# Optimization experiments

Hardware: AMD Instinct MI355X
Metric: run time of the kernel (lower is better)

The kernel has to match this reference:

```python
import jax, jax.numpy as jnp
import numpy as np

E = 8        # n_routed_experts
K = 4        # num_experts_per_tok
T = 1024     # tokens
H = 1024     # hidden_size
I = 1408     # moe_intermediate_size


def setup_inputs() -> dict:
    key = jax.random.key(0)
    ks = jax.random.split(key, 6)
    hidden_states = jax.random.normal(ks[0], (T, H), jnp.float32)
    rw = jax.random.uniform(ks[1], (T, K), jnp.float32)
    router_weights = rw / jnp.sum(rw, axis=-1, keepdims=True)  # normalized top-k router weights
    selected_experts = jax.random.randint(ks[2], (T, K), 0, E, jnp.int32)
    gate_w = jax.random.normal(ks[3], (E, H, I), jnp.float32) * (H ** -0.5)  # lecun_normal-ish
    up_w = jax.random.normal(ks[4], (E, H, I), jnp.float32) * (H ** -0.5)
    down_w = jax.random.normal(ks[5], (E, I, H), jnp.float32) * (I ** -0.5)
    return {
        'hidden_states': hidden_states,
        'router_weights': router_weights,
        'gate_w': gate_w,
        'up_w': up_w,
        'down_w': down_w,
        'selected_experts': selected_experts,
    }


def _grouped_matmul(x, w, seg):
    # x: [m, k] tokens sorted by expert; w: [E, k, n]; seg: [m] expert id per row.
    # Grouped GEMM expressed as E masked GEMMs (fixed small loop over experts);
    # a custom kernel would do true variable-group-size grouped GEMM.
    out = jnp.zeros((x.shape[0], w.shape[-1]), x.dtype)
    for e in range(w.shape[0]):
        out = out + jnp.where((seg == e)[:, None], x, jnp.zeros((), x.dtype)) @ w[e]
    return out


def reference(hidden_states, router_weights, gate_w, up_w, down_w, selected_experts):
    t, k = selected_experts.shape
    flat = selected_experts.ravel()                       # [t*k]
    hs = jnp.repeat(hidden_states, k, axis=0)             # [t*k, H]
    sort_idx = jnp.argsort(flat)                          # dispatch: sort tokens by expert
    seg = flat[sort_idx]
    xs = hs[sort_idx]
    gate = _grouped_matmul(xs, gate_w, seg)               # [t*k, I]
    up = _grouped_matmul(xs, up_w, seg)                   # [t*k, I]
    h = jax.nn.silu(gate) * up                            # fused SwiGLU
    down = _grouped_matmul(h, down_w, seg)                # [t*k, H]
    unsort = jnp.argsort(sort_idx)                        # scatter back to token order
    out = down[unsort].reshape(t, k, -1)
    return jnp.sum(out * router_weights[..., None], axis=1)  # weighted combine [t, H]
```

## Files before the change

kernel.cpp:

```cpp
#include <hip/hip_runtime.h>
#include <hip/hip_bf16.h>
#include <cstdint>
#include <cstddef>

#define NE 8
#define NT 1024
#define NK 4
#define NH 1024
#define NI 1408
#define NA (NT * NK)
#define BM 128
#define MAXTILES 40
#define PADSLOTS 5120

typedef short short8 __attribute__((ext_vector_type(8)));
typedef float f32x4 __attribute__((ext_vector_type(4)));
typedef float f4v __attribute__((ext_vector_type(4)));
typedef unsigned short u16;

#define WS_HDR   0
#define WS_SORT  1024
#define WS_XBF   21504
#define WS_GT    2118656
#define WS_UT    25187328
#define WS_DT    48256000
#define WS_HB    71324672

__device__ __forceinline__ u16 f2b(float f) {
  union { float f; uint32_t u; } c; c.f = f;
  uint32_t u = c.u;
  return (u16)((u + 0x7FFFu + ((u >> 16) & 1u)) >> 16);
}

__device__ __forceinline__ void llds16(const void* g, void* l) {
  __builtin_amdgcn_global_load_lds(
      (const __attribute__((address_space(1))) void*)g,
      (__attribute__((address_space(3))) void*)l, 16, 0, 0);
}

__device__ __forceinline__ void transcvt_stripe(const float* __restrict__ src,
                                                u16* __restrict__ dst,
                                                int K, int N, int k0, int n0,
                                                u16* smem, int tid) {
  u16 (*t2)[64][64] = (u16(*)[64][64])smem;
  int r = tid >> 4, c = tid & 15;
  f4v v[2][4];
#pragma unroll
  for (int t = 0; t < 2; ++t)
#pragma unroll
    for (int i = 0; i < 4; ++i)
      v[t][i] = __builtin_nontemporal_load(
          (const f4v*)&src[(size_t)(k0 + r + 16 * i) * N + n0 + t * 64 + c * 4]);
#pragma unroll
  for (int t = 0; t < 2; ++t)
#pragma unroll
    for (int i = 0; i < 4; ++i) {
      ushort4 o;
      o.x = f2b(v[t][i].x); o.y = f2b(v[t][i].y); o.z = f2b(v[t][i].z); o.w = f2b(v[t][i].w);
      int row = r + 16 * i;
      int sc = (c * 4) ^ (row & 56);
      *(ushort4*)&t2[t][row][sc] = o;
    }
  __syncthreads();
#pragma unroll
  for (int t = 0; t < 2; ++t)
#pragma unroll
    for (int i = 0; i < 2; ++i) {
      int idx = i * 256 + tid;
      int n = idx >> 3, kc = idx & 7;
      int cs = n ^ (kc * 8);
      u16 o[8];
#pragma unroll
      for (int j = 0; j < 8; ++j) o[j] = t2[t][kc * 8 + j][cs];
      *(short8*)&dst[(size_t)(n0 + t * 64 + n) * K + k0 + kc * 8] = *(const short8*)o;
    }
}

__global__ __launch_bounds__(256) void k1_prep(
    const float* __restrict__ gw, const float* __restrict__ uw, const float* __restrict__ dw,
    const float* __restrict__ hs, const int* __restrict__ sel,
    u16* __restrict__ gT, u16* __restrict__ uT, u16* __restrict__ dT, u16* __restrict__ xbf,
    int* __restrict__ hdr, int* __restrict__ sorted, float* __restrict__ outz) {
  int tid = threadIdx.x;
  int y = blockIdx.y;
  if (y == 24) {
    for (int i = blockIdx.x * 256 + tid; i * 4 < NT * NH; i += 176 * 256) {
      f4v v = __builtin_nontemporal_load((const f4v*)&hs[i * 4]);
      ushort4 o;
      o.x = f2b(v.x); o.y = f2b(v.y); o.z = f2b(v.z); o.w = f2b(v.w);
      *(ushort4*)&xbf[i * 4] = o;
    }
    return;
  }
  if (y == 25) {
    int x = blockIdx.x;
    if (x >= 1 && x <= 64) {
      int base = (x - 1) * 16384;
      f4v z = {0.f, 0.f, 0.f, 0.f};
#pragma unroll
      for (int i = 0; i < 16; ++i)
        *(f4v*)&outz[base + (i * 256 + tid) * 4] = z;
      return;
    }
    if (x != 0) return;
    __shared__ int cnt[NE], fill[NE], poff_s[NE + 1];
    if (tid < NE) { cnt[tid] = 0; fill[tid] = 0; }
    __syncthreads();
    for (int i = tid; i < NA; i += 256) atomicAdd(&cnt[sel[i]], 1);
    __syncthreads();
    if (tid == 0) {
      int off = 0, nt = 0;
      for (int e = 0; e < NE; ++e) {
        poff_s[e] = off;
        int tiles = (cnt[e] + BM - 1) / BM;
        for (int j = 0; j < tiles; ++j) { hdr[32 + nt] = e; hdr[80 + nt] = off + j * BM; ++nt; }
        off += tiles * BM;
      }
      poff_s[NE] = off;
      hdr[17] = nt;
      for (int e = 0; e < NE; ++e) hdr[e] = cnt[e];
      for (int e = 0; e <= NE; ++e) hdr[8 + e] = poff_s[e];
    }
    __syncthreads();
    for (int i = tid; i < PADSLOTS; i += 256) sorted[i] = -1;
    __syncthreads();
    for (int i = tid; i < NA; i += 256) {
      int e = sel[i];
      int p = atomicAdd(&fill[e], 1);
      sorted[poff_s[e] + p] = i;
    }
    return;
  }
  __shared__ u16 smem[2 * 64 * 64];
  if (y < 16) {
    int tensor = y >> 3, e = y & 7;
    const float* src = ((tensor == 0) ? gw : uw) + (size_t)e * NH * NI;
    u16* dst = ((tensor == 0) ? gT : uT) + (size_t)e * NH * NI;
    int nb = blockIdx.x % 11, kb = blockIdx.x / 11;
    transcvt_stripe(src, dst, NH, NI, kb * 64, nb * 128, smem, tid);
  } else {
    int e = y - 16;
    const float* src = dw + (size_t)e * NI * NH;
    u16* dst = dT + (size_t)e * NI * NH;
    int nb = blockIdx.x % 8, kb = blockIdx.x / 8;
    transcvt_stripe(src, dst, NI, NH, kb * 64, nb * 128, smem, tid);
  }
}

__global__ __launch_bounds__(256, 2) void k2_gemm1(
    const u16* __restrict__ xbf, const u16* __restrict__ gT, const u16* __restrict__ uT,
    u16* __restrict__ hbuf, const int* __restrict__ hdr, const int* __restrict__ sorted) {
  __shared__ u16 smem[24576];
  int b = blockIdx.x;
  int tid = threadIdx.x;

  int tile = b % 40;
  if (tile >= hdr[17]) return;
  int e = hdr[32 + tile];
  int slot0 = hdr[80 + tile];
  int n0 = (b / 40) * 128;

  u16* sA  = smem;
  u16* sBg = smem + 8192;
  u16* sBu = smem + 16384;

  const u16* aptr[4];
  for (int s = 0; s < 4; ++s) {
    int idx = s * 256 + tid;
    int row = idx >> 3, c = idx & 7;
    int kc = c ^ (row & 7);
    int as = sorted[slot0 + row];
    int trow = (as >= 0) ? (as >> 2) : 0;
    aptr[s] = xbf + (size_t)trow * NH + kc * 8;
  }
  const u16 *bgp[4], *bup[4];
  for (int s = 0; s < 4; ++s) {
    int idx = s * 256 + tid;
    int n = idx >> 3, c = idx & 7;
    int kc = c ^ (n & 7);
    size_t o = ((size_t)e * NI + n0 + n) * NH + kc * 8;
    bgp[s] = gT + o; bup[s] = uT + o;
  }

  int lane = tid & 63, wave = tid >> 6;
  int wm = wave >> 1, wn = wave & 1;
  int l15 = lane & 15, quad = lane >> 4;
  int sw = l15 & 7;

  f32x4 accg[4][4] = {}; f32x4 accu[4][4] = {};

  for (int kt = 0; kt < NH / 64; ++kt) {
    int ko = kt * 64;
    for (int s = 0; s < 4; ++s) llds16(aptr[s] + ko, &sA[(s * 256 + tid) * 8]);
    for (int s = 0; s < 4; ++s) llds16(bgp[s] + ko, &sBg[(s * 256 + tid) * 8]);
    for (int s = 0; s < 4; ++s) llds16(bup[s] + ko, &sBu[(s * 256 + tid) * 8]);
    __syncthreads();
    for (int ks = 0; ks < 2; ++ks) {
      int pos = ((ks * 4 + quad) ^ sw) * 8;
      short8 av[4], bg[4], bu[4];
      for (int mf = 0; mf < 4; ++mf)
        av[mf] = *(const short8*)&sA[(wm * 64 + mf * 16 + l15) * 64 + pos];
      for (int nf = 0; nf < 4; ++nf) {
        bg[nf] = *(const short8*)&sBg[(wn * 64 + nf * 16 + l15) * 64 + pos];
        bu[nf] = *(const short8*)&sBu[(wn * 64 + nf * 16 + l15) * 64 + pos];
      }
      for (int mf = 0; mf < 4; ++mf)
        for (int nf = 0; nf < 4; ++nf) {
          accg[mf][nf] = __builtin_amdgcn_mfma_f32_16x16x32_bf16(av[mf], bg[nf], accg[mf][nf], 0, 0, 0);
          accu[mf][nf] = __builtin_amdgcn_mfma_f32_16x16x32_bf16(av[mf], bu[nf], accu[mf][nf], 0, 0, 0);
        }
    }
    __syncthreads();
  }

  for (int mf = 0; mf < 4; ++mf)
    for (int nf = 0; nf < 4; ++nf)
      for (int r = 0; r < 4; ++r) {
        int row = wm * 64 + mf * 16 + quad * 4 + r;
        int col = n0 + wn * 64 + nf * 16 + l15;
        float g2 = accg[mf][nf][r], u = accu[mf][nf][r];
        float hv = (g2 / (1.f + __expf(-g2))) * u;
        hbuf[(size_t)(slot0 + row) * NI + col] = f2b(hv);
      }
}

__global__ __launch_bounds__(256, 4) void k3_gemm2(
    const u16* __restrict__ hbuf, const u16* __restrict__ dT,
    const float* __restrict__ rw, float* __restrict__ out,
    const int* __restrict__ hdr, const int* __restrict__ sorted) {
  int tile = blockIdx.x;
  if (tile >= hdr[17]) return;
  int e = hdr[32 + tile];
  int slot0 = hdr[80 + tile];
  int n0 = blockIdx.y * 128;
  int tid = threadIdx.x;

  __shared__ u16 sA[128 * 64];
  __shared__ u16 sB[128 * 64];

  const u16 *ap[4], *bp[4];
  for (int s = 0; s < 4; ++s) {
    int idx = s * 256 + tid;
    int r = idx >> 3, c = idx & 7;
    int kc = c ^ (r & 7);
    ap[s] = hbuf + (size_t)(slot0 + r) * NI + kc * 8;
    bp[s] = dT + ((size_t)e * NH + n0 + r) * NI + kc * 8;
  }

  int lane = tid & 63, wave = tid >> 6;
  int wm = wave >> 1, wn = wave & 1;
  int l15 = lane & 15, quad = lane >> 4;
  int sw = l15 & 7;

  f32x4 acc[4][4] = {};

  for (int kt = 0; kt < NI / 64; ++kt) {
    int ko = kt * 64;
    for (int s = 0; s < 4; ++s) llds16(ap[s] + ko, &sA[(s * 256 + tid) * 8]);
    for (int s = 0; s < 4; ++s) llds16(bp[s] + ko, &sB[(s * 256 + tid) * 8]);
    __syncthreads();
    for (int ks = 0; ks < 2; ++ks) {
      int pos = ((ks * 4 + quad) ^ sw) * 8;
      short8 av[4], bv[4];
      for (int mf = 0; mf < 4; ++mf)
        av[mf] = *(const short8*)&sA[(wm * 64 + mf * 16 + l15) * 64 + pos];
      for (int nf = 0; nf < 4; ++nf)
        bv[nf] = *(const short8*)&sB[(wn * 64 + nf * 16 + l15) * 64 + pos];
      for (int mf = 0; mf < 4; ++mf)
        for (int nf = 0; nf < 4; ++nf)
          acc[mf][nf] = __builtin_amdgcn_mfma_f32_16x16x32_bf16(av[mf], bv[nf], acc[mf][nf], 0, 0, 0);
    }
    __syncthreads();
  }

  for (int mf = 0; mf < 4; ++mf) {
    int rowb = wm * 64 + mf * 16 + quad * 4;
    for (int r = 0; r < 4; ++r) {
      int as = sorted[slot0 + rowb + r];
      if (as < 0) continue;
      float w = rw[as];
      float* orow = out + (size_t)(as >> 2) * NH + n0 + wn * 64;
      for (int nf = 0; nf < 4; ++nf)
        atomicAdd(&orow[nf * 16 + l15], w * acc[mf][nf][r]);
    }
  }
}

extern "C" void kernel_launch(void* const* d_in, const int* in_sizes, int n_in,
                              void* d_out, int out_size, void* d_ws, size_t ws_size,
                              hipStream_t stream) {
  const float* hs  = (const float*)d_in[0];
  const float* rw  = (const float*)d_in[1];
  const float* gw  = (const float*)d_in[2];
  const float* uw  = (const float*)d_in[3];
  const float* dw  = (const float*)d_in[4];
  const int*   sel = (const int*)d_in[5];
  float* out = (float*)d_out;

  char* ws = (char*)d_ws;
  int*  hdr    = (int*)(ws + WS_HDR);
  int*  sorted = (int*)(ws + WS_SORT);
  u16*  xbf    = (u16*)(ws + WS_XBF);
  u16*  gT     = (u16*)(ws + WS_GT);
  u16*  uT     = (u16*)(ws + WS_UT);
  u16*  dT     = (u16*)(ws + WS_DT);
  u16*  hb     = (u16*)(ws + WS_HB);

  hipLaunchKernelGGL(k1_prep, dim3(176, 26), dim3(256), 0, stream,
                     gw, uw, dw, hs, sel, gT, uT, dT, xbf, hdr, sorted, out);
  hipLaunchKernelGGL(k2_gemm1, dim3(440), dim3(256), 0, stream,
                     xbf, gT, uT, hb, hdr, sorted);
  hipLaunchKernelGGL(k3_gemm2, dim3(MAXTILES, NH / 128), dim3(256), 0, stream,
                     hb, dT, rw, out, hdr, sorted);
}
```

Measured before the change: 246.2 us.

## Triple-buffer LDS with async prefetch two stages ahead in both GEMMs

Both grouped GEMM kernels switch from a single-buffered load, sync, compute loop with K-step 64 to a three-stage LDS ring with K-step 32. Direct-to-LDS loads are issued two stages ahead and gated by explicit vmcnt waits plus a single barrier per iteration, so global latency overlaps MFMA work. The swizzle is reworked for 32-wide rows. LDS use grows, and the second GEMM's launch bounds drop from 4 to 3 blocks per CU, which may reduce occupancy.

```diff
diff --git a/kernel.cpp b/kernel.cpp
--- a/kernel.cpp
+++ b/kernel.cpp
@@ -150,7 +150,7 @@
 __global__ __launch_bounds__(256, 2) void k2_gemm1(
     const u16* __restrict__ xbf, const u16* __restrict__ gT, const u16* __restrict__ uT,
     u16* __restrict__ hbuf, const int* __restrict__ hdr, const int* __restrict__ sorted) {
-  __shared__ u16 smem[24576];
+  __shared__ u16 smem[36864];
   int b = blockIdx.x;
   int tid = threadIdx.x;
 
@@ -160,58 +160,68 @@
   int slot0 = hdr[80 + tile];
   int n0 = (b / 40) * 128;
 
-  u16* sA  = smem;
-  u16* sBg = smem + 8192;
-  u16* sBu = smem + 16384;
-
-  const u16* aptr[4];
-  for (int s = 0; s < 4; ++s) {
+  const u16* aptr[2];
+  const u16 *bgp[2], *bup[2];
+#pragma unroll
+  for (int s = 0; s < 2; ++s) {
     int idx = s * 256 + tid;
-    int row = idx >> 3, c = idx & 7;
-    int kc = c ^ (row & 7);
+    int row = idx >> 2, c = idx & 3;
+    int kc = c ^ (row & 3) ^ ((row >> 2) & 3);
     int as = sorted[slot0 + row];
     int trow = (as >= 0) ? (as >> 2) : 0;
     aptr[s] = xbf + (size_t)trow * NH + kc * 8;
-  }
-  const u16 *bgp[4], *bup[4];
-  for (int s = 0; s < 4; ++s) {
-    int idx = s * 256 + tid;
-    int n = idx >> 3, c = idx & 7;
-    int kc = c ^ (n & 7);
-    size_t o = ((size_t)e * NI + n0 + n) * NH + kc * 8;
+    size_t o = ((size_t)e * NI + n0 + row) * NH + kc * 8;
     bgp[s] = gT + o; bup[s] = uT + o;
   }
 
   int lane = tid & 63, wave = tid >> 6;
   int wm = wave >> 1, wn = wave & 1;
   int l15 = lane & 15, quad = lane >> 4;
-  int sw = l15 & 7;
+  int pos = ((quad ^ (l15 & 3) ^ ((l15 >> 2) & 3)) & 3) * 8;
 
   f32x4 accg[4][4] = {}; f32x4 accu[4][4] = {};
 
-  for (int kt = 0; kt < NH / 64; ++kt) {
-    int ko = kt * 64;
-    for (int s = 0; s < 4; ++s) llds16(aptr[s] + ko, &sA[(s * 256 + tid) * 8]);
-    for (int s = 0; s < 4; ++s) llds16(bgp[s] + ko, &sBg[(s * 256 + tid) * 8]);
-    for (int s = 0; s < 4; ++s) llds16(bup[s] + ko, &sBu[(s * 256 + tid) * 8]);
-    __syncthreads();
-    for (int ks = 0; ks < 2; ++ks) {
-      int pos = ((ks * 4 + quad) ^ sw) * 8;
-      short8 av[4], bg[4], bu[4];
-      for (int mf = 0; mf < 4; ++mf)
-        av[mf] = *(const short8*)&sA[(wm * 64 + mf * 16 + l15) * 64 + pos];
+#define K2_STAGE(BUF, KT)                                                \
+  {                                                                      \
+    int ko_ = (KT) * 32;                                                 \
+    u16* p_ = smem + (BUF) * 12288;                                      \
+    llds16(aptr[0] + ko_, p_ + tid * 8);                                 \
+    llds16(aptr[1] + ko_, p_ + (256 + tid) * 8);                         \
+    llds16(bgp[0] + ko_, p_ + 4096 + tid * 8);                           \
+    llds16(bgp[1] + ko_, p_ + 4096 + (256 + tid) * 8);                   \
+    llds16(bup[0] + ko_, p_ + 8192 + tid * 8);                           \
+    llds16(bup[1] + ko_, p_ + 8192 + (256 + tid) * 8);                   \
+  }
+
+  K2_STAGE(0, 0);
+  K2_STAGE(1, 1);
+  for (int kt = 0; kt < 32; ++kt) {
+    if (kt == 31) { asm volatile("s_waitcnt vmcnt(0)" ::: "memory"); }
+    else          { asm volatile("s_waitcnt vmcnt(6)" ::: "memory"); }
+    __builtin_amdgcn_s_barrier();
+    __builtin_amdgcn_sched_barrier(0);
+    if (kt < 30) K2_STAGE((kt + 2) % 3, kt + 2);
+    const u16* sA  = smem + (kt % 3) * 12288;
+    const u16* sBg = sA + 4096;
+    const u16* sBu = sA + 8192;
+    short8 av[4], bg[4], bu[4];
+#pragma unroll
+    for (int mf = 0; mf < 4; ++mf)
+      av[mf] = *(const short8*)&sA[(wm * 64 + mf * 16 + l15) * 32 + pos];
+#pragma unroll
+    for (int nf = 0; nf < 4; ++nf) {
+      bg[nf] = *(const short8*)&sBg[(wn * 64 + nf * 16 + l15) * 32 + pos];
+      bu[nf] = *(const short8*)&sBu[(wn * 64 + nf * 16 + l15) * 32 + pos];
+    }
+#pragma unroll
+    for (int mf = 0; mf < 4; ++mf)
+#pragma unroll
       for (int nf = 0; nf < 4; ++nf) {
-        bg[nf] = *(const short8*)&sBg[(wn * 64 + nf * 16 + l15) * 64 + pos];
-        bu[nf] = *(const short8*)&sBu[(wn * 64 + nf * 16 + l15) * 64 + pos];
+        accg[mf][nf] = __builtin_amdgcn_mfma_f32_16x16x32_bf16(av[mf], bg[nf], accg[mf][nf], 0, 0, 0);
+        accu[mf][nf] = __builtin_amdgcn_mfma_f32_16x16x32_bf16(av[mf], bu[nf], accu[mf][nf], 0, 0, 0);
       }
-      for (int mf = 0; mf < 4; ++mf)
-        for (int nf = 0; nf < 4; ++nf) {
-          accg[mf][nf] = __builtin_amdgcn_mfma_f32_16x16x32_bf16(av[mf], bg[nf], accg[mf][nf], 0, 0, 0);
-          accu[mf][nf] = __builtin_amdgcn_mfma_f32_16x16x32_bf16(av[mf], bu[nf], accu[mf][nf], 0, 0, 0);
-        }
-    }
-    __syncthreads();
-  }
+  }
+#undef K2_STAGE
 
   for (int mf = 0; mf < 4; ++mf)
     for (int nf = 0; nf < 4; ++nf)
@@ -224,10 +234,11 @@
       }
 }
 
-__global__ __launch_bounds__(256, 4) void k3_gemm2(
+__global__ __launch_bounds__(256, 3) void k3_gemm2(
     const u16* __restrict__ hbuf, const u16* __restrict__ dT,
     const float* __restrict__ rw, float* __restrict__ out,
     const int* __restrict__ hdr, const int* __restrict__ sorted) {
+  __shared__ u16 smem[24576];
   int tile = blockIdx.x;
   if (tile >= hdr[17]) return;
   int e = hdr[32 + tile];
@@ -235,43 +246,57 @@
   int n0 = blockIdx.y * 128;
   int tid = threadIdx.x;
 
-  __shared__ u16 sA[128 * 64];
-  __shared__ u16 sB[128 * 64];
-
-  const u16 *ap[4], *bp[4];
-  for (int s = 0; s < 4; ++s) {
+  const u16 *ap[2], *bp[2];
+#pragma unroll
+  for (int s = 0; s < 2; ++s) {
     int idx = s * 256 + tid;
-    int r = idx >> 3, c = idx & 7;
-    int kc = c ^ (r & 7);
-    ap[s] = hbuf + (size_t)(slot0 + r) * NI + kc * 8;
-    bp[s] = dT + ((size_t)e * NH + n0 + r) * NI + kc * 8;
+    int row = idx >> 2, c = idx & 3;
+    int kc = c ^ (row & 3) ^ ((row >> 2) & 3);
+    ap[s] = hbuf + (size_t)(slot0 + row) * NI + kc * 8;
+    bp[s] = dT + ((size_t)e * NH + n0 + row) * NI + kc * 8;
   }
 
   int lane = tid & 63, wave = tid >> 6;
   int wm = wave >> 1, wn = wave & 1;
   int l15 = lane & 15, quad = lane >> 4;
-  int sw = l15 & 7;
+  int pos = ((quad ^ (l15 & 3) ^ ((l15 >> 2) & 3)) & 3) * 8;
 
   f32x4 acc[4][4] = {};
 
-  for (int kt = 0; kt < NI / 64; ++kt) {
-    int ko = kt * 64;
-    for (int s = 0; s < 4; ++s) llds16(ap[s] + ko, &sA[(s * 256 + tid) * 8]);
-    for (int s = 0; s < 4; ++s) llds16(bp[s] + ko, &sB[(s * 256 + tid) * 8]);
-    __syncthreads();
-    for (int ks = 0; ks < 2; ++ks) {
-      int pos = ((ks * 4 + quad) ^ sw) * 8;
-      short8 av[4], bv[4];
-      for (int mf = 0; mf < 4; ++mf)
-        av[mf] = *(const short8*)&sA[(wm * 64 + mf * 16 + l15) * 64 + pos];
+#define K3_STAGE(BUF, KT)                                                \
+  {                                                                      \
+    int ko_ = (KT) * 32;                                                 \
+    u16* p_ = smem + (BUF) * 8192;                                       \
+    llds16(ap[0] + ko_, p_ + tid * 8);                                   \
+    llds16(ap[1] + ko_, p_ + (256 + tid) * 8);                           \
+    llds16(bp[0] + ko_, p_ + 4096 + tid * 8);                            \
+    llds16(bp[1] + ko_, p_ + 4096 + (256 + tid) * 8);                    \
+  }
+
+  K3_STAGE(0, 0);
+  K3_STAGE(1, 1);
+  for (int kt = 0; kt < 44; ++kt) {
+    if (kt == 43) { asm volatile("s_waitcnt vmcnt(0)" ::: "memory"); }
+    else          { asm volatile("s_waitcnt vmcnt(4)" ::: "memory"); }
+    __builtin_amdgcn_s_barrier();
+    __builtin_amdgcn_sched_barrier(0);
+    if (kt < 42) K3_STAGE((kt + 2) % 3, kt + 2);
+    const u16* sA = smem + (kt % 3) * 8192;
+    const u16* sB = sA + 4096;
+    short8 av[4], bv[4];
+#pragma unroll
+    for (int mf = 0; mf < 4; ++mf)
+      av[mf] = *(const short8*)&sA[(wm * 64 + mf * 16 + l15) * 32 + pos];
+#pragma unroll
+    for (int nf = 0; nf < 4; ++nf)
+      bv[nf] = *(const short8*)&sB[(wn * 64 + nf * 16 + l15) * 32 + pos];
+#pragma unroll
+    for (int mf = 0; mf < 4; ++mf)
+#pragma unroll
       for (int nf = 0; nf < 4; ++nf)
-        bv[nf] = *(const short8*)&sB[(wn * 64 + nf * 16 + l15) * 64 + pos];
-      for (int mf = 0; mf < 4; ++mf)
-        for (int nf = 0; nf < 4; ++nf)
-          acc[mf][nf] = __builtin_amdgcn_mfma_f32_16x16x32_bf16(av[mf], bv[nf], acc[mf][nf], 0, 0, 0);
-    }
-    __syncthreads();
-  }
+        acc[mf][nf] = __builtin_amdgcn_mfma_f32_16x16x32_bf16(av[mf], bv[nf], acc[mf][nf], 0, 0, 0);
+  }
+#undef K3_STAGE
 
   for (int mf = 0; mf < 4; ++mf) {
     int rowb = wm * 64 + mf * 16 + quad * 4;
```

New measurement: 247.9 us. No clear change (+0.7%).
